# Optimization experiments

Hardware: AMD Instinct MI355X
Metric: run time of the kernel (lower is better)

## Reference

```python
import jax, jax.numpy as jnp
from jax import lax
import numpy as np

N, E, G, CPG = 4096, 16, 14, 8  # wafers, experts, groups (wafer sub-arrays), channels per group
C = G * CPG  # 112


def setup_inputs() -> dict:
    key = jax.random.key(0)
    ks = jax.random.split(key, 9)
    s = 0.05
    x = jax.random.normal(ks[0], (N, G, 8, 8), jnp.float32)
    keys = jax.random.randint(ks[1], (N,), 0, E)
    # hexagonal wafer conv mask (buffer in the torch module); corners zeroed
    conv_mask = jnp.array([[1.0, 1.0, 0.0], [1.0, 1.0, 1.0], [0.0, 1.0, 1.0]], jnp.float32)
    enc_conv_w = jax.random.normal(ks[2], (E, C, 1, 3, 3), jnp.float32) * s
    enc_dense_w = jax.random.normal(ks[3], (E, G, 8, 128), jnp.float32) * s
    enc_dense_b = jax.random.normal(ks[4], (E, G, 8), jnp.float32) * s
    dec_dense_w = jax.random.normal(ks[5], (E, G, 128, 8), jnp.float32) * s
    dec_dense_b = jax.random.normal(ks[6], (E, G, 128), jnp.float32) * s
    dec_tconv_w = jax.random.normal(ks[7], (E, C, 1, 3, 3), jnp.float32) * s
    dec_tconv_b = jax.random.normal(ks[8], (E, G), jnp.float32) * s
    return dict(x=x, keys=keys, conv_mask=conv_mask,
                enc_conv_w=enc_conv_w, enc_dense_w=enc_dense_w, enc_dense_b=enc_dense_b,
                dec_dense_w=dec_dense_w, dec_dense_b=dec_dense_b,
                dec_tconv_w=dec_tconv_w, dec_tconv_b=dec_tconv_b)


def reference(x, keys, conv_mask, enc_conv_w, enc_dense_w, enc_dense_b,
              dec_dense_w, dec_dense_b, dec_tconv_w, dec_tconv_b):
    n = x.shape[0]
    dn = ('NCHW', 'OIHW', 'NCHW')

    # ---- encoder: masked grouped conv (bias=False) ----
    wc = enc_conv_w[keys] * conv_mask  # [N,112,1,3,3]; mask broadcasts over spatial taps

    def enc_conv(xi, wi):
        return lax.conv_general_dilated(xi[None], wi, (1, 1), 'SAME',
                                        feature_group_count=G, dimension_numbers=dn)[0]

    h = jax.nn.relu(jax.vmap(enc_conv)(x, wc))           # [N,112,8,8]
    h = h.reshape(n, C, 4, 2, 4, 2).max(axis=(3, 5))     # MaxPool2d(2) -> [N,112,4,4]
    feat = h.reshape(n, G, CPG * 16)                      # [N,14,128] (group-major, matches torch view)
    z = jax.nn.relu(jnp.einsum('ngof,ngf->ngo', enc_dense_w[keys], feat) + enc_dense_b[keys])  # [N,14,8]

    # ---- decoder ----
    y = jax.nn.relu(jnp.einsum('ngfo,ngo->ngf', dec_dense_w[keys], z) + dec_dense_b[keys])  # [N,14,128]
    y = y.reshape(n, C, 4, 4)

    # ConvTranspose2d(112,14,3,stride=2,pad=1,outpad=1,groups=14) as a dilated forward conv
    # with spatially flipped kernels: per group, 8 in -> 1 out.
    wt = jnp.flip(dec_tconv_w[keys].reshape(n, G, CPG, 3, 3), axis=(-2, -1))  # [N,14,8,3,3] OIHW
    bt = dec_tconv_b[keys]  # [N,14]

    def dec_tconv(yi, wi, bi):
        o = lax.conv_general_dilated(yi[None], wi, (1, 1), ((1, 2), (1, 2)),
                                     lhs_dilation=(2, 2), feature_group_count=G,
                                     dimension_numbers=dn)[0]
        return o + bi[:, None, None]

    out = jax.vmap(dec_tconv)(y, wt, bt)  # [N,14,8,8]
    return jax.nn.relu(out)
```

## Files before the change

### kernel.cpp

```cpp
#include <hip/hip_runtime.h>
#include <hip/hip_fp16.h>

#define NG 14
#define NE 16
#define NW 32
#define YW 152

typedef __fp16 h2 __attribute__((ext_vector_type(2)));
typedef __fp16 h4 __attribute__((ext_vector_type(4)));
typedef __fp16 h8 __attribute__((ext_vector_type(8)));

__device__ __forceinline__ float hdot4(h4 a, h4 b, float c) {
    const h2 a0 = __builtin_shufflevector(a, a, 0, 1);
    const h2 a1 = __builtin_shufflevector(a, a, 2, 3);
    const h2 b0 = __builtin_shufflevector(b, b, 0, 1);
    const h2 b1 = __builtin_shufflevector(b, b, 2, 3);
    return __builtin_amdgcn_fdot2(a1, b1, __builtin_amdgcn_fdot2(a0, b0, c, false), false);
}

__global__ __launch_bounds__(1024) void bin_kernel(const int* __restrict__ keys, int N,
                                                   int NBW, int* __restrict__ sorted) {
    __shared__ int hist[NE], offs[NE], cur[NE];
    __shared__ int runTot;
    const int t = threadIdx.x;
    if (t < NE) { hist[t] = 0; cur[t] = 0; }
    __syncthreads();
    for (int i = t; i < N; i += 1024) atomicAdd(&hist[keys[i]], 1);
    __syncthreads();
    if (t == 0) {
        int run = 0;
        for (int e = 0; e < NE; ++e) { offs[e] = run; run += (hist[e] + NW - 1) & ~(NW - 1); }
        runTot = run;
    }
    __syncthreads();
    for (int i = t; i < N; i += 1024) {
        const int e = keys[i];
        sorted[offs[e] + atomicAdd(&cur[e], 1)] = i;
    }
    {
        const int e = t >> 6, l = t & 63;
        const int cnt = hist[e];
        const int padded = (cnt + NW - 1) & ~(NW - 1);
        if (l < padded - cnt) sorted[offs[e] + cnt + l] = -1;
    }
    for (int i = runTot + t; i < NBW; i += 1024) sorted[i] = -1;
}

#define XEL(R,C) (((R) < 0 || (R) > 7 || (C) < 0 || (C) > 7) ? 0.f : xv[(R)&7][(C)&7])

__global__ __launch_bounds__(256, 4) void ae_main(
    const float* __restrict__ x,
    const int*   __restrict__ keys,
    const float* __restrict__ conv_mask,
    const float* __restrict__ enc_conv_w,
    const float* __restrict__ enc_dense_w,
    const float* __restrict__ enc_dense_b,
    const float* __restrict__ dec_dense_w,
    const float* __restrict__ dec_dense_b,
    const float* __restrict__ dec_tconv_w,
    const float* __restrict__ dec_tconv_b,
    const int*   __restrict__ sorted,
    float* __restrict__ out)
{
    const int t = threadIdx.x;
    const int chunk = blockIdx.x / NG;
    const int g = blockIdx.x - chunk * NG;

    __shared__ __attribute__((aligned(16))) __half yt[NW * YW];
    __shared__ __attribute__((aligned(16))) h2 ews2[640];
    __shared__ __attribute__((aligned(16))) h2 dws2[512];
    __shared__ __attribute__((aligned(16))) h2 wtr2[48];
    __shared__ __attribute__((aligned(16))) float wcs[72];
    __shared__ float dbs[128];
    __shared__ float ebs[8];

    const int* chunkIds = sorted + chunk * NW;
    const int i0 = chunkIds[0];
    if (i0 < 0) return;
    const int k = keys[i0];

    const int w = t >> 3, ch = t & 7;
    const int idw = chunkIds[w];
    const int idr = (idw < 0) ? i0 : idw;

    const float* xg = x + (size_t)idr * 896 + g * 64;
    float xv[8][8];
    #pragma unroll
    for (int r = 0; r < 8; ++r) {
        const float4 a = *(const float4*)(xg + r * 8);
        const float4 b = *(const float4*)(xg + r * 8 + 4);
        xv[r][0]=a.x; xv[r][1]=a.y; xv[r][2]=a.z; xv[r][3]=a.w;
        xv[r][4]=b.x; xv[r][5]=b.y; xv[r][6]=b.z; xv[r][7]=b.w;
    }

    const size_t wg1024 = (size_t)(k * NG + g) * 1024;
    {
        const float4 w4 = *(const float4*)(enc_dense_w + wg1024 + 4 * t);
        const int o = t >> 5, c2 = (t >> 2) & 7, pr = t & 3;
        const int base = (pr * 8 + c2) * 20 + o * 2;
        ews2[base]     = __builtin_amdgcn_cvt_pkrtz(w4.x, w4.y);
        ews2[base + 1] = __builtin_amdgcn_cvt_pkrtz(w4.z, w4.w);
    }
    if (t < 128) {
        const float4 a = *(const float4*)(dec_dense_w + wg1024 + 8 * t);
        const float4 b = *(const float4*)(dec_dense_w + wg1024 + 8 * t + 4);
        const int c2 = t >> 4, p = t & 15;
        h2* dst = &dws2[(p * 8 + c2) * 4];
        dst[0] = __builtin_amdgcn_cvt_pkrtz(a.x, a.y);
        dst[1] = __builtin_amdgcn_cvt_pkrtz(a.z, a.w);
        dst[2] = __builtin_amdgcn_cvt_pkrtz(b.x, b.y);
        dst[3] = __builtin_amdgcn_cvt_pkrtz(b.z, b.w);
    } else if (t < 200) {
        const int i = t - 128, c2 = i / 9, tap = i - c2 * 9;
        wcs[tap * 8 + c2] = enc_conv_w[(size_t)k * 1008 + (g * 8 + c2) * 9 + tap] * conv_mask[tap];
    } else if (t < 208) {
        ebs[t - 200] = enc_dense_b[(size_t)k * 112 + g * 8 + (t - 200)];
    } else if (t < 256) {
        const int i = t - 208, tap = i >> 2, j = i & 3;
        h2 v = (h2)(__fp16)0.f;
        if (tap < 9) {
            const float wa = dec_tconv_w[(size_t)k * 1008 + (g * 8 + 2*j) * 9 + tap];
            const float wb = dec_tconv_w[(size_t)k * 1008 + (g * 8 + 2*j + 1) * 9 + tap];
            v = __builtin_amdgcn_cvt_pkrtz(wa, wb);
        }
        wtr2[tap * 4 + j] = v;
    }
    if (t < 128) {
        dbs[(t & 15) * 8 + (t >> 4)] = dec_dense_b[(size_t)k * 1792 + g * 128 + t];
    }
    __syncthreads();

    const float w0 = wcs[0*8+ch], w1 = wcs[1*8+ch], w3 = wcs[3*8+ch], w4 = wcs[4*8+ch],
                w5 = wcs[5*8+ch], w7 = wcs[7*8+ch], w8 = wcs[8*8+ch];
    float part[8] = {0.f,0.f,0.f,0.f,0.f,0.f,0.f,0.f};
    #pragma unroll
    for (int pr = 0; pr < 4; ++pr) {
        float res[4];
        #pragma unroll
        for (int pc = 0; pc < 4; ++pc) {
            float mx = 0.f;
            #pragma unroll
            for (int rl = 0; rl < 2; ++rl) {
                #pragma unroll
                for (int cl = 0; cl < 2; ++cl) {
                    const int ir = 2*pr + rl, jc = 2*pc + cl;
                    const float s = w0*XEL(ir-1,jc-1) + w1*XEL(ir-1,jc)
                                  + w3*XEL(ir,jc-1)  + w4*XEL(ir,jc) + w5*XEL(ir,jc+1)
                                  + w7*XEL(ir+1,jc)  + w8*XEL(ir+1,jc+1);
                    mx = fmaxf(mx, s);
                }
            }
            res[pc] = mx;
        }
        const h2 ra = __builtin_amdgcn_cvt_pkrtz(res[0], res[1]);
        const h2 rb = __builtin_amdgcn_cvt_pkrtz(res[2], res[3]);
        const h2* eb2 = &ews2[(pr * 8 + ch) * 20];
        #pragma unroll
        for (int q = 0; q < 4; ++q) {
            const h8 v = *(const h8*)(eb2 + q * 4);
            const h2 a0 = __builtin_shufflevector(v, v, 0, 1);
            const h2 a1 = __builtin_shufflevector(v, v, 2, 3);
            const h2 b0 = __builtin_shufflevector(v, v, 4, 5);
            const h2 b1 = __builtin_shufflevector(v, v, 6, 7);
            part[2*q]   = __builtin_amdgcn_fdot2(rb, a1, __builtin_amdgcn_fdot2(ra, a0, part[2*q],   false), false);
            part[2*q+1] = __builtin_amdgcn_fdot2(rb, b1, __builtin_amdgcn_fdot2(ra, b0, part[2*q+1], false), false);
        }
    }

    float z[8];
    #pragma unroll
    for (int o = 0; o < 8; ++o) {
        float v = part[o];
        v += __shfl_xor(v, 1);
        v += __shfl_xor(v, 2);
        v += __shfl_xor(v, 4);
        z[o] = fmaxf(v + ebs[o], 0.f);
    }
    const h2 z01 = __builtin_amdgcn_cvt_pkrtz(z[0], z[1]);
    const h2 z23 = __builtin_amdgcn_cvt_pkrtz(z[2], z[3]);
    const h2 z45 = __builtin_amdgcn_cvt_pkrtz(z[4], z[5]);
    const h2 z67 = __builtin_amdgcn_cvt_pkrtz(z[6], z[7]);

    __half* yw_ = yt + w * YW;
    #pragma unroll
    for (int p = 0; p < 16; ++p) {
        const h8 v = *(const h8*)(&dws2[(p * 8 + ch) * 4]);
        const h2 v0 = __builtin_shufflevector(v, v, 0, 1);
        const h2 v1 = __builtin_shufflevector(v, v, 2, 3);
        const h2 v2 = __builtin_shufflevector(v, v, 4, 5);
        const h2 v3 = __builtin_shufflevector(v, v, 6, 7);
        float acc = dbs[p * 8 + ch];
        acc = __builtin_amdgcn_fdot2(z01, v0, acc, false);
        acc = __builtin_amdgcn_fdot2(z23, v1, acc, false);
        acc = __builtin_amdgcn_fdot2(z45, v2, acc, false);
        acc = __builtin_amdgcn_fdot2(z67, v3, acc, false);
        yw_[(p >> 2) * 40 + (p & 3) * 8 + ch] = __float2half(fmaxf(acc, 0.f));
    }
    asm volatile("s_waitcnt lgkmcnt(0)" ::: "memory");

    const int oi = ch;
    int iA, rA, iB, rB;
    if ((oi & 1) == 0) { iA = oi >> 1; rA = 3; iB = 0; rB = 9; }
    else { iA = (oi - 1) >> 1; rA = 6;
           if (oi < 7) { iB = (oi + 1) >> 1; rB = 0; } else { iB = 0; rB = 9; } }
    const float bias = dec_tconv_b[k * NG + g];
    const __fp16* ywh = (const __fp16*)(yt) + w * YW;

    h8 yAv[4], yBv[4];
    #pragma unroll
    for (int j = 0; j < 4; ++j) {
        yAv[j] = *(const h8*)(ywh + iA * 40 + j * 8);
        yBv[j] = *(const h8*)(ywh + iB * 40 + j * 8);
    }
    float acc[8] = {0.f,0.f,0.f,0.f,0.f,0.f,0.f,0.f};
    #pragma unroll
    for (int hc = 0; hc < 2; ++hc) {
        const h4 wA0 = *(const h4*)(wtr2 + (rA + 0) * 4 + hc * 2);
        const h4 wA1 = *(const h4*)(wtr2 + (rA + 1) * 4 + hc * 2);
        const h4 wA2 = *(const h4*)(wtr2 + (rA + 2) * 4 + hc * 2);
        const h4 wB0 = *(const h4*)(wtr2 + (rB + 0) * 4 + hc * 2);
        const h4 wB1 = *(const h4*)(wtr2 + (rB + 1) * 4 + hc * 2);
        const h4 wB2 = *(const h4*)(wtr2 + (rB + 2) * 4 + hc * 2);
        h4 yA[4], yB[4];
        #pragma unroll
        for (int j = 0; j < 4; ++j) {
            yA[j] = hc ? __builtin_shufflevector(yAv[j], yAv[j], 4, 5, 6, 7)
                       : __builtin_shufflevector(yAv[j], yAv[j], 0, 1, 2, 3);
            yB[j] = hc ? __builtin_shufflevector(yBv[j], yBv[j], 4, 5, 6, 7)
                       : __builtin_shufflevector(yBv[j], yBv[j], 0, 1, 2, 3);
        }
        acc[0] = hdot4(wB1, yB[0], hdot4(wA1, yA[0], acc[0]));
        acc[1] = hdot4(wB0, yB[1], hdot4(wB2, yB[0],
                 hdot4(wA0, yA[1], hdot4(wA2, yA[0], acc[1]))));
        acc[2] = hdot4(wB1, yB[1], hdot4(wA1, yA[1], acc[2]));
        acc[3] = hdot4(wB0, yB[2], hdot4(wB2, yB[1],
                 hdot4(wA0, yA[2], hdot4(wA2, yA[1], acc[3]))));
        acc[4] = hdot4(wB1, yB[2], hdot4(wA1, yA[2], acc[4]));
        acc[5] = hdot4(wB0, yB[3], hdot4(wB2, yB[2],
                 hdot4(wA0, yA[3], hdot4(wA2, yA[2], acc[5]))));
        acc[6] = hdot4(wB1, yB[3], hdot4(wA1, yA[3], acc[6]));
        acc[7] = hdot4(wB2, yB[3], hdot4(wA2, yA[3], acc[7]));
    }
    if (idw >= 0) {
        float* og = out + (size_t)idw * 896 + g * 64 + oi * 8;
        *(float4*)(og)     = make_float4(fmaxf(acc[0]+bias,0.f), fmaxf(acc[1]+bias,0.f),
                                         fmaxf(acc[2]+bias,0.f), fmaxf(acc[3]+bias,0.f));
        *(float4*)(og + 4) = make_float4(fmaxf(acc[4]+bias,0.f), fmaxf(acc[5]+bias,0.f),
                                         fmaxf(acc[6]+bias,0.f), fmaxf(acc[7]+bias,0.f));
    }
}

extern "C" void kernel_launch(void* const* d_in, const int* in_sizes, int n_in,
                              void* d_out, int out_size, void* d_ws, size_t ws_size,
                              hipStream_t stream) {
    const float* x            = (const float*)d_in[0];
    const int*   keys         = (const int*)d_in[1];
    const float* conv_mask    = (const float*)d_in[2];
    const float* enc_conv_w   = (const float*)d_in[3];
    const float* enc_dense_w  = (const float*)d_in[4];
    const float* enc_dense_b  = (const float*)d_in[5];
    const float* dec_dense_w  = (const float*)d_in[6];
    const float* dec_dense_b  = (const float*)d_in[7];
    const float* dec_tconv_w  = (const float*)d_in[8];
    const float* dec_tconv_b  = (const float*)d_in[9];
    float* out = (float*)d_out;

    const int N = in_sizes[0] / (NG * 64);
    const int CHUNKS = (N + NE * (NW - 1)) / NW + 1;
    int* sorted = (int*)d_ws;

    bin_kernel<<<1, 1024, 0, stream>>>(keys, N, CHUNKS * NW, sorted);
    ae_main<<<CHUNKS * NG, 256, 0, stream>>>(
        x, keys, conv_mask, enc_conv_w, enc_dense_w, enc_dense_b,
        dec_dense_w, dec_dense_b, dec_tconv_w, dec_tconv_b, sorted, out);
}
```

Measured before the change: 27.10 us.

## Parallelize key binning across experts and vectorize decoder dense with swizzled LDS

The binning kernel now runs one block per expert instead of a single 1024-thread block. Each block recomputes the histogram, finds its own offset and scatters only its own indices, so scattering and padding are spread across blocks. In exchange every block reads the full keys array and rebuilds the whole histogram. The decoder dense layer now has each lane compute 8 consecutive output channels for two spatial positions and write them as one h8 store. The dec_dense weights are stored with an XOR swizzle in LDS to avoid bank conflicts.

```diff
diff --git a/kernel.cpp b/kernel.cpp
--- a/kernel.cpp
+++ b/kernel.cpp
@@ -18,32 +18,29 @@
     return __builtin_amdgcn_fdot2(a1, b1, __builtin_amdgcn_fdot2(a0, b0, c, false), false);
 }
 
-__global__ __launch_bounds__(1024) void bin_kernel(const int* __restrict__ keys, int N,
-                                                   int NBW, int* __restrict__ sorted) {
-    __shared__ int hist[NE], offs[NE], cur[NE];
-    __shared__ int runTot;
+__global__ __launch_bounds__(256) void bin_kernel(const int* __restrict__ keys, int N,
+                                                  int NBW, int* __restrict__ sorted) {
+    __shared__ int hist[NE];
+    __shared__ int cur;
+    const int e = blockIdx.x;
     const int t = threadIdx.x;
-    if (t < NE) { hist[t] = 0; cur[t] = 0; }
+    if (t < NE) hist[t] = 0;
+    if (t == 0) cur = 0;
     __syncthreads();
-    for (int i = t; i < N; i += 1024) atomicAdd(&hist[keys[i]], 1);
+    for (int i = t; i < N; i += 256) atomicAdd(&hist[keys[i]], 1);
     __syncthreads();
-    if (t == 0) {
-        int run = 0;
-        for (int e = 0; e < NE; ++e) { offs[e] = run; run += (hist[e] + NW - 1) & ~(NW - 1); }
-        runTot = run;
-    }
-    __syncthreads();
-    for (int i = t; i < N; i += 1024) {
-        const int e = keys[i];
-        sorted[offs[e] + atomicAdd(&cur[e], 1)] = i;
-    }
-    {
-        const int e = t >> 6, l = t & 63;
-        const int cnt = hist[e];
-        const int padded = (cnt + NW - 1) & ~(NW - 1);
-        if (l < padded - cnt) sorted[offs[e] + cnt + l] = -1;
-    }
-    for (int i = runTot + t; i < NBW; i += 1024) sorted[i] = -1;
+    int off = 0;
+    #pragma unroll
+    for (int e2 = 0; e2 < NE; ++e2) if (e2 < e) off += (hist[e2] + NW - 1) & ~(NW - 1);
+    const int cnt = hist[e];
+    const int padded = (cnt + NW - 1) & ~(NW - 1);
+    for (int i = t; i < N; i += 256) {
+        if (keys[i] == e) sorted[off + atomicAdd(&cur, 1)] = i;
+    }
+    for (int i = cnt + t; i < padded; i += 256) sorted[off + i] = -1;
+    if (e == NE - 1) {
+        for (int i = off + padded + t; i < NBW; i += 256) sorted[i] = -1;
+    }
 }
 
 #define XEL(R,C) (((R) < 0 || (R) > 7 || (C) < 0 || (C) > 7) ? 0.f : xv[(R)&7][(C)&7])
@@ -105,7 +102,7 @@
         const float4 a = *(const float4*)(dec_dense_w + wg1024 + 8 * t);
         const float4 b = *(const float4*)(dec_dense_w + wg1024 + 8 * t + 4);
         const int c2 = t >> 4, p = t & 15;
-        h2* dst = &dws2[(p * 8 + c2) * 4];
+        h2* dst = &dws2[(p * 8 + (c2 ^ (p & 7))) * 4];
         dst[0] = __builtin_amdgcn_cvt_pkrtz(a.x, a.y);
         dst[1] = __builtin_amdgcn_cvt_pkrtz(a.z, a.w);
         dst[2] = __builtin_amdgcn_cvt_pkrtz(b.x, b.y);
@@ -183,18 +180,31 @@
 
     __half* yw_ = yt + w * YW;
     #pragma unroll
-    for (int p = 0; p < 16; ++p) {
-        const h8 v = *(const h8*)(&dws2[(p * 8 + ch) * 4]);
-        const h2 v0 = __builtin_shufflevector(v, v, 0, 1);
-        const h2 v1 = __builtin_shufflevector(v, v, 2, 3);
-        const h2 v2 = __builtin_shufflevector(v, v, 4, 5);
-        const h2 v3 = __builtin_shufflevector(v, v, 6, 7);
-        float acc = dbs[p * 8 + ch];
-        acc = __builtin_amdgcn_fdot2(z01, v0, acc, false);
-        acc = __builtin_amdgcn_fdot2(z23, v1, acc, false);
-        acc = __builtin_amdgcn_fdot2(z45, v2, acc, false);
-        acc = __builtin_amdgcn_fdot2(z67, v3, acc, false);
-        yw_[(p >> 2) * 40 + (p & 3) * 8 + ch] = __float2half(fmaxf(acc, 0.f));
+    for (int pp = 0; pp < 2; ++pp) {
+        const int p = ch + pp * 8;
+        const int px = p & 7;
+        const float4 db0 = *(const float4*)(dbs + p * 8);
+        const float4 db1 = *(const float4*)(dbs + p * 8 + 4);
+        const float dbv[8] = {db0.x, db0.y, db0.z, db0.w, db1.x, db1.y, db1.z, db1.w};
+        __fp16 yv[8];
+        #pragma unroll
+        for (int c = 0; c < 8; ++c) {
+            const h8 v = *(const h8*)(&dws2[(p * 8 + (c ^ px)) * 4]);
+            const h2 v0 = __builtin_shufflevector(v, v, 0, 1);
+            const h2 v1 = __builtin_shufflevector(v, v, 2, 3);
+            const h2 v2 = __builtin_shufflevector(v, v, 4, 5);
+            const h2 v3 = __builtin_shufflevector(v, v, 6, 7);
+            float acc = dbv[c];
+            acc = __builtin_amdgcn_fdot2(z01, v0, acc, false);
+            acc = __builtin_amdgcn_fdot2(z23, v1, acc, false);
+            acc = __builtin_amdgcn_fdot2(z45, v2, acc, false);
+            acc = __builtin_amdgcn_fdot2(z67, v3, acc, false);
+            yv[c] = (__fp16)fmaxf(acc, 0.f);
+        }
+        h8 o8;
+        #pragma unroll
+        for (int c = 0; c < 8; ++c) o8[c] = yv[c];
+        *(h8*)(yw_ + (p >> 2) * 40 + (p & 3) * 8) = o8;
     }
     asm volatile("s_waitcnt lgkmcnt(0)" ::: "memory");
 
@@ -269,7 +279,7 @@
     const int CHUNKS = (N + NE * (NW - 1)) / NW + 1;
     int* sorted = (int*)d_ws;
 
-    bin_kernel<<<1, 1024, 0, stream>>>(keys, N, CHUNKS * NW, sorted);
+    bin_kernel<<<NE, 256, 0, stream>>>(keys, N, CHUNKS * NW, sorted);
     ae_main<<<CHUNKS * NG, 256, 0, stream>>>(
         x, keys, conv_mask, enc_conv_w, enc_dense_w, enc_dense_b,
         dec_dense_w, dec_dense_b, dec_tconv_w, dec_tconv_b, sorted, out);
```

New measurement: 30.78 us. 13.6% more time.
